# Kernel optimization log

Measured on AMD Instinct MI355X. Metric: run time of the kernel, lower is better.

The kernel has to match this reference:

```python
import jax, jax.numpy as jnp
import numpy as np

MASK_VALUE = -1000000.0  # matches torch source's value=-1000000.0


def setup_inputs() -> dict:
    key = jax.random.key(0)
    kq, kk, kv, kl = jax.random.split(key, 4)
    B, S, D = 64, 1024, 64
    q = jax.random.normal(kq, (B, S, D), dtype=jnp.float32)
    k = jax.random.normal(kk, (B, S, D), dtype=jnp.float32)
    v = jax.random.normal(kv, (B, S, D), dtype=jnp.float32)
    valid_lens = jax.random.randint(kl, (B,), 0, S, dtype=jnp.int32)
    return {"q": q, "k": k, "v": v, "valid_lens": valid_lens}


def reference(q, k, v, valid_lens):
    # scores: [B, Sq, Sk]
    d = q.shape[-1]
    scores = jnp.einsum("bqd,bkd->bqk", q, k) / jnp.sqrt(jnp.float32(d))
    # 1-D valid_lens broadcast over the query dim (torch repeat_interleave branch)
    Sk = k.shape[1]
    mask = jnp.arange(Sk, dtype=jnp.int32)[None, None, :] < valid_lens[:, None, None]
    scores = jnp.where(mask, scores, MASK_VALUE)
    attn = jax.nn.softmax(scores, axis=-1)
    # dropout p=0.0 -> identity (eval-mode reference)
    return jnp.einsum("bqk,bkd->bqd", attn, v)
```

## Files before the change

kernel.cpp:

```cpp
#include <hip/hip_runtime.h>
#include <math.h>


#define BATCH 64
#define SEQ   1024
#define DIM   64
#define BQ    64
#define BC    64
#define NKT   (SEQ / BC)
#define LSTR  72
#define QSCALE 0.18033688011112442f
#define MASKED -1.0e6f

typedef __attribute__((ext_vector_type(8))) short bf16x8;
typedef __attribute__((ext_vector_type(4))) float f32x4;

__device__ __forceinline__ uint pack2_trunc(float lo, float hi) {
    return __builtin_amdgcn_perm(__float_as_uint(hi), __float_as_uint(lo), 0x07060302);
}
__device__ __forceinline__ ushort f2bf_rne(float x) {
    uint u = __float_as_uint(x);
    return (ushort)((u + 0x7fffu + ((u >> 16) & 1u)) >> 16);
}

__global__ __launch_bounds__(256, 4) void attn_mfma_flash2(
    const float* __restrict__ q, const float* __restrict__ k,
    const float* __restrict__ v, const int* __restrict__ valid_lens,
    float* __restrict__ out)
{
    __shared__ ushort Ks[BC * LSTR];
    __shared__ ushort Vt[DIM * LSTR];
    __shared__ ushort Ps[BQ * LSTR];

    const int t    = threadIdx.x;
    const int wave = t >> 6;
    const int wl   = t & 63;
    const int QD   = wl >> 4;
    const int li   = wl & 15;
    const int b    = blockIdx.x & 63;
    const int q0   = (blockIdx.x >> 6) * BQ;
    const int vl   = valid_lens[b];

    const size_t boff = (size_t)b * SEQ * DIM;

    bf16x8 qb[2];
    {
        const float* qrow = q + boff + (size_t)(q0 + wave * 16 + li) * DIM + QD * 8;
        #pragma unroll
        for (int kc = 0; kc < 2; kc++) {
            float4 a = *(const float4*)(qrow + kc * 32);
            float4 c = *(const float4*)(qrow + kc * 32 + 4);
            union { bf16x8 v; ushort u[8]; } tmp;
            tmp.u[0] = f2bf_rne(a.x * QSCALE);
            tmp.u[1] = f2bf_rne(a.y * QSCALE);
            tmp.u[2] = f2bf_rne(a.z * QSCALE);
            tmp.u[3] = f2bf_rne(a.w * QSCALE);
            tmp.u[4] = f2bf_rne(c.x * QSCALE);
            tmp.u[5] = f2bf_rne(c.y * QSCALE);
            tmp.u[6] = f2bf_rne(c.z * QSCALE);
            tmp.u[7] = f2bf_rne(c.w * QSCALE);
            qb[kc] = tmp.v;
        }
    }

    const int it_max = (vl == 0) ? NKT : ((vl + BC - 1) >> 6);

    float4 kf[4];
    float  vf[2][8];

    auto load_tile = [&](int it) {
        const float4* kg = (const float4*)(k + boff + (size_t)it * BC * DIM);
        #pragma unroll
        for (int i = 0; i < 4; i++) kf[i] = kg[t + 256 * i];
        const float* vgf = v + boff + (size_t)it * BC * DIM;
        #pragma unroll
        for (int i = 0; i < 2; i++) {
            int slot = t + 256 * i;
            int d = slot & 63, ko = slot >> 6;
            #pragma unroll
            for (int j = 0; j < 8; j++)
                vf[i][j] = vgf[(size_t)(ko * 8 + j) * DIM + d];
        }
    };

    auto stage = [&]() {
        #pragma unroll
        for (int i = 0; i < 4; i++) {
            int idx = t + 256 * i;
            int row = idx >> 4, c4 = idx & 15;
            uint2 w;
            w.x = pack2_trunc(kf[i].x, kf[i].y);
            w.y = pack2_trunc(kf[i].z, kf[i].w);
            *(uint2*)&Ks[row * LSTR + c4 * 4] = w;
        }
        #pragma unroll
        for (int i = 0; i < 2; i++) {
            int slot = t + 256 * i;
            int d = slot & 63, ko = slot >> 6;
            uint4 w;
            w.x = pack2_trunc(vf[i][0], vf[i][1]);
            w.y = pack2_trunc(vf[i][2], vf[i][3]);
            w.z = pack2_trunc(vf[i][4], vf[i][5]);
            w.w = pack2_trunc(vf[i][6], vf[i][7]);
            *(uint4*)&Vt[d * LSTR + ko * 8] = w;
        }
    };

    float m_run = -INFINITY, l_run = 0.f;
    f32x4 acc[4];
    #pragma unroll
    for (int dt = 0; dt < 4; dt++) acc[dt] = (f32x4){0.f, 0.f, 0.f, 0.f};

    load_tile(0);

    for (int it = 0; it < it_max; it++) {
        __syncthreads();
        stage();
        if (it + 1 < it_max) load_tile(it + 1);
        __syncthreads();

        f32x4 sc[4];
        #pragma unroll
        for (int kt = 0; kt < 4; kt++) {
            bf16x8 ka0 = *(const bf16x8*)&Ks[(kt * 16 + li) * LSTR + QD * 8];
            bf16x8 ka1 = *(const bf16x8*)&Ks[(kt * 16 + li) * LSTR + 32 + QD * 8];
            f32x4 c = (f32x4){0.f, 0.f, 0.f, 0.f};
            c = __builtin_amdgcn_mfma_f32_16x16x32_bf16(ka0, qb[0], c, 0, 0, 0);
            c = __builtin_amdgcn_mfma_f32_16x16x32_bf16(ka1, qb[1], c, 0, 0, 0);
            sc[kt] = c;
        }

        const int kbase = it * BC;
        if (kbase + BC > vl) {
            #pragma unroll
            for (int kt = 0; kt < 4; kt++)
                #pragma unroll
                for (int r = 0; r < 4; r++) {
                    int key = kbase + kt * 16 + QD * 4 + r;
                    if (key >= vl) sc[kt][r] = MASKED;
                }
        }

        float mt = -INFINITY;
        #pragma unroll
        for (int kt = 0; kt < 4; kt++)
            #pragma unroll
            for (int r = 0; r < 4; r++) mt = fmaxf(mt, sc[kt][r]);
        mt = fmaxf(mt, __shfl_xor(mt, 16, 64));
        mt = fmaxf(mt, __shfl_xor(mt, 32, 64));
        float mn = fmaxf(m_run, mt);
        float alpha = exp2f(m_run - mn);
        m_run = mn;

        float ls = 0.f;
        #pragma unroll
        for (int kt = 0; kt < 4; kt++) {
            float p0 = exp2f(sc[kt][0] - mn);
            float p1 = exp2f(sc[kt][1] - mn);
            float p2 = exp2f(sc[kt][2] - mn);
            float p3 = exp2f(sc[kt][3] - mn);
            ls += (p0 + p1) + (p2 + p3);
            uint2 w;
            w.x = pack2_trunc(p0, p1);
            w.y = pack2_trunc(p2, p3);
            *(uint2*)&Ps[(wave * 16 + li) * LSTR + kt * 16 + QD * 4] = w;
        }
        ls += __shfl_xor(ls, 16, 64);
        ls += __shfl_xor(ls, 32, 64);
        l_run = l_run * alpha + ls;

        float a0 = __shfl(alpha, QD * 4 + 0, 64);
        float a1 = __shfl(alpha, QD * 4 + 1, 64);
        float a2 = __shfl(alpha, QD * 4 + 2, 64);
        float a3 = __shfl(alpha, QD * 4 + 3, 64);
        #pragma unroll
        for (int dt = 0; dt < 4; dt++) {
            acc[dt][0] *= a0; acc[dt][1] *= a1;
            acc[dt][2] *= a2; acc[dt][3] *= a3;
        }

        bf16x8 pa0 = *(const bf16x8*)&Ps[(wave * 16 + li) * LSTR + QD * 8];
        bf16x8 pa1 = *(const bf16x8*)&Ps[(wave * 16 + li) * LSTR + 32 + QD * 8];
        #pragma unroll
        for (int dt = 0; dt < 4; dt++) {
            bf16x8 vb0 = *(const bf16x8*)&Vt[(dt * 16 + li) * LSTR + QD * 8];
            bf16x8 vb1 = *(const bf16x8*)&Vt[(dt * 16 + li) * LSTR + 32 + QD * 8];
            acc[dt] = __builtin_amdgcn_mfma_f32_16x16x32_bf16(pa0, vb0, acc[dt], 0, 0, 0);
            acc[dt] = __builtin_amdgcn_mfma_f32_16x16x32_bf16(pa1, vb1, acc[dt], 0, 0, 0);
        }
    }

    float invl = 1.0f / l_run;
    float i0 = __shfl(invl, QD * 4 + 0, 64);
    float i1 = __shfl(invl, QD * 4 + 1, 64);
    float i2 = __shfl(invl, QD * 4 + 2, 64);
    float i3 = __shfl(invl, QD * 4 + 3, 64);
    float* ob = out + boff + (size_t)q0 * DIM;
    const int rbase = wave * 16 + QD * 4;
    #pragma unroll
    for (int dt = 0; dt < 4; dt++) {
        int col = dt * 16 + li;
        ob[(size_t)(rbase + 0) * DIM + col] = acc[dt][0] * i0;
        ob[(size_t)(rbase + 1) * DIM + col] = acc[dt][1] * i1;
        ob[(size_t)(rbase + 2) * DIM + col] = acc[dt][2] * i2;
        ob[(size_t)(rbase + 3) * DIM + col] = acc[dt][3] * i3;
    }
}

extern "C" void kernel_launch(void* const* d_in, const int* in_sizes, int n_in,
                              void* d_out, int out_size, void* d_ws, size_t ws_size,
                              hipStream_t stream) {
    const float* q = (const float*)d_in[0];
    const float* k = (const float*)d_in[1];
    const float* v = (const float*)d_in[2];
    const int* valid_lens = (const int*)d_in[3];
    float* out = (float*)d_out;

    dim3 grid(BATCH * (SEQ / BQ));
    dim3 block(256);
    attn_mfma_flash2<<<grid, block, 0, stream>>>(q, k, v, valid_lens, out);
}
```

Baseline: 127.5 us.

## Use persistent blocks with atomic work queue and smaller double-buffered key tiles

The kernel becomes persistent: 768 blocks pull (batch, query-tile) items from a global atomic counter instead of launching one block per item. This balances the uneven per-batch work that variable valid_lens creates. The key tile shrinks from 64 to 32, and K/V fragments are read into registers before the barrier so the next tile can be staged while MFMAs run, giving a two-deep prefetch. The cost is an extra memset launch, the atomic traffic, more barriers per key, and lower occupancy from launch bounds of 3.

```diff
diff --git a/kernel.cpp b/kernel.cpp
--- a/kernel.cpp
+++ b/kernel.cpp
@@ -6,9 +6,13 @@
 #define SEQ   1024
 #define DIM   64
 #define BQ    64
-#define BC    64
+#define BC    32
 #define NKT   (SEQ / BC)
-#define LSTR  72
+#define KSTR  72
+#define VSTR  40
+#define PSTR  40
+#define NITEMS (BATCH * (SEQ / BQ))
+#define GRID  768
 #define QSCALE 0.18033688011112442f
 #define MASKED -1.0e6f
 
@@ -23,187 +27,191 @@
     return (ushort)((u + 0x7fffu + ((u >> 16) & 1u)) >> 16);
 }
 
-__global__ __launch_bounds__(256, 4) void attn_mfma_flash2(
+__global__ __launch_bounds__(256, 3) void attn_mfma_flash4(
     const float* __restrict__ q, const float* __restrict__ k,
     const float* __restrict__ v, const int* __restrict__ valid_lens,
-    float* __restrict__ out)
+    float* __restrict__ out, unsigned* __restrict__ cnt)
 {
-    __shared__ ushort Ks[BC * LSTR];
-    __shared__ ushort Vt[DIM * LSTR];
-    __shared__ ushort Ps[BQ * LSTR];
+    __shared__ ushort Ks[BC * KSTR];
+    __shared__ ushort Vt[DIM * VSTR];
+    __shared__ ushort Ps[BQ * PSTR];
+    __shared__ int next_item;
 
     const int t    = threadIdx.x;
     const int wave = t >> 6;
     const int wl   = t & 63;
     const int QD   = wl >> 4;
     const int li   = wl & 15;
-    const int b    = blockIdx.x & 63;
-    const int q0   = (blockIdx.x >> 6) * BQ;
-    const int vl   = valid_lens[b];
-
-    const size_t boff = (size_t)b * SEQ * DIM;
-
-    bf16x8 qb[2];
-    {
-        const float* qrow = q + boff + (size_t)(q0 + wave * 16 + li) * DIM + QD * 8;
+
+    int item = blockIdx.x;
+    while (item < NITEMS) {
+        const int b  = item & 63;
+        const int q0 = (item >> 6) * BQ;
+        const int vl = valid_lens[b];
+        const size_t boff = (size_t)b * SEQ * DIM;
+
+        bf16x8 qb[2];
+        {
+            const float* qrow = q + boff + (size_t)(q0 + wave * 16 + li) * DIM + QD * 8;
+            #pragma unroll
+            for (int kc = 0; kc < 2; kc++) {
+                float4 a = *(const float4*)(qrow + kc * 32);
+                float4 c = *(const float4*)(qrow + kc * 32 + 4);
+                union { bf16x8 v; ushort u[8]; } tmp;
+                tmp.u[0] = f2bf_rne(a.x * QSCALE);
+                tmp.u[1] = f2bf_rne(a.y * QSCALE);
+                tmp.u[2] = f2bf_rne(a.z * QSCALE);
+                tmp.u[3] = f2bf_rne(a.w * QSCALE);
+                tmp.u[4] = f2bf_rne(c.x * QSCALE);
+                tmp.u[5] = f2bf_rne(c.y * QSCALE);
+                tmp.u[6] = f2bf_rne(c.z * QSCALE);
+                tmp.u[7] = f2bf_rne(c.w * QSCALE);
+                qb[kc] = tmp.v;
+            }
+        }
+
+        const int it_max = (vl == 0) ? NKT : ((vl + BC - 1) / BC);
+
+        float4 kf[2];
+        float  vf[8];
+
+        auto load_tile = [&](int it) {
+            const float4* kg = (const float4*)(k + boff + (size_t)it * BC * DIM);
+            kf[0] = kg[t];
+            kf[1] = kg[t + 256];
+            const float* vgf = v + boff + (size_t)it * BC * DIM;
+            #pragma unroll
+            for (int j = 0; j < 8; j++)
+                vf[j] = vgf[(size_t)(wave * 8 + j) * DIM + wl];
+        };
+        auto stage = [&]() {
+            #pragma unroll
+            for (int i = 0; i < 2; i++) {
+                int idx = t + 256 * i;
+                int row = idx >> 4, c4 = idx & 15;
+                uint2 w;
+                w.x = pack2_trunc(kf[i].x, kf[i].y);
+                w.y = pack2_trunc(kf[i].z, kf[i].w);
+                *(uint2*)&Ks[row * KSTR + c4 * 4] = w;
+            }
+            uint4 wv;
+            wv.x = pack2_trunc(vf[0], vf[1]);
+            wv.y = pack2_trunc(vf[2], vf[3]);
+            wv.z = pack2_trunc(vf[4], vf[5]);
+            wv.w = pack2_trunc(vf[6], vf[7]);
+            *(uint4*)&Vt[wl * VSTR + wave * 8] = wv;
+        };
+
+        float m_run = -INFINITY, l_run = 0.f;
+        f32x4 acc[4];
         #pragma unroll
-        for (int kc = 0; kc < 2; kc++) {
-            float4 a = *(const float4*)(qrow + kc * 32);
-            float4 c = *(const float4*)(qrow + kc * 32 + 4);
-            union { bf16x8 v; ushort u[8]; } tmp;
-            tmp.u[0] = f2bf_rne(a.x * QSCALE);
-            tmp.u[1] = f2bf_rne(a.y * QSCALE);
-            tmp.u[2] = f2bf_rne(a.z * QSCALE);
-            tmp.u[3] = f2bf_rne(a.w * QSCALE);
-            tmp.u[4] = f2bf_rne(c.x * QSCALE);
-            tmp.u[5] = f2bf_rne(c.y * QSCALE);
-            tmp.u[6] = f2bf_rne(c.z * QSCALE);
-            tmp.u[7] = f2bf_rne(c.w * QSCALE);
-            qb[kc] = tmp.v;
+        for (int dt = 0; dt < 4; dt++) acc[dt] = (f32x4){0.f, 0.f, 0.f, 0.f};
+
+        load_tile(0);
+        stage();
+        if (it_max > 1) load_tile(1);
+        __syncthreads();
+
+        for (int it = 0; it < it_max; it++) {
+            bf16x8 ka[2][2], vb[4];
+            #pragma unroll
+            for (int kt = 0; kt < 2; kt++) {
+                ka[kt][0] = *(const bf16x8*)&Ks[(kt * 16 + li) * KSTR + QD * 8];
+                ka[kt][1] = *(const bf16x8*)&Ks[(kt * 16 + li) * KSTR + 32 + QD * 8];
+            }
+            #pragma unroll
+            for (int dt = 0; dt < 4; dt++)
+                vb[dt] = *(const bf16x8*)&Vt[(dt * 16 + li) * VSTR + QD * 8];
+            __syncthreads();
+
+            if (it + 1 < it_max) stage();
+            if (it + 2 < it_max) load_tile(it + 2);
+
+            f32x4 sc[2];
+            #pragma unroll
+            for (int kt = 0; kt < 2; kt++) {
+                f32x4 c = (f32x4){0.f, 0.f, 0.f, 0.f};
+                c = __builtin_amdgcn_mfma_f32_16x16x32_bf16(ka[kt][0], qb[0], c, 0, 0, 0);
+                c = __builtin_amdgcn_mfma_f32_16x16x32_bf16(ka[kt][1], qb[1], c, 0, 0, 0);
+                sc[kt] = c;
+            }
+
+            const int kbase = it * BC;
+            if (kbase + BC > vl) {
+                #pragma unroll
+                for (int kt = 0; kt < 2; kt++)
+                    #pragma unroll
+                    for (int r = 0; r < 4; r++) {
+                        int key = kbase + kt * 16 + QD * 4 + r;
+                        if (key >= vl) sc[kt][r] = MASKED;
+                    }
+            }
+
+            float mt = -INFINITY;
+            #pragma unroll
+            for (int kt = 0; kt < 2; kt++)
+                #pragma unroll
+                for (int r = 0; r < 4; r++) mt = fmaxf(mt, sc[kt][r]);
+            mt = fmaxf(mt, __shfl_xor(mt, 16, 64));
+            mt = fmaxf(mt, __shfl_xor(mt, 32, 64));
+            float mn = fmaxf(m_run, mt);
+            float alpha = exp2f(m_run - mn);
+            m_run = mn;
+
+            float ls = 0.f;
+            #pragma unroll
+            for (int kt = 0; kt < 2; kt++) {
+                float p0 = exp2f(sc[kt][0] - mn);
+                float p1 = exp2f(sc[kt][1] - mn);
+                float p2 = exp2f(sc[kt][2] - mn);
+                float p3 = exp2f(sc[kt][3] - mn);
+                ls += (p0 + p1) + (p2 + p3);
+                uint2 w;
+                w.x = pack2_trunc(p0, p1);
+                w.y = pack2_trunc(p2, p3);
+                *(uint2*)&Ps[(wave * 16 + li) * PSTR + kt * 16 + QD * 4] = w;
+            }
+            ls += __shfl_xor(ls, 16, 64);
+            ls += __shfl_xor(ls, 32, 64);
+            l_run = l_run * alpha + ls;
+
+            float a0 = __shfl(alpha, QD * 4 + 0, 64);
+            float a1 = __shfl(alpha, QD * 4 + 1, 64);
+            float a2 = __shfl(alpha, QD * 4 + 2, 64);
+            float a3 = __shfl(alpha, QD * 4 + 3, 64);
+            #pragma unroll
+            for (int dt = 0; dt < 4; dt++) {
+                acc[dt][0] *= a0; acc[dt][1] *= a1;
+                acc[dt][2] *= a2; acc[dt][3] *= a3;
+            }
+
+            bf16x8 pa = *(const bf16x8*)&Ps[(wave * 16 + li) * PSTR + QD * 8];
+            #pragma unroll
+            for (int dt = 0; dt < 4; dt++)
+                acc[dt] = __builtin_amdgcn_mfma_f32_16x16x32_bf16(pa, vb[dt], acc[dt], 0, 0, 0);
+
+            __syncthreads();
         }
-    }
-
-    const int it_max = (vl == 0) ? NKT : ((vl + BC - 1) >> 6);
-
-    float4 kf[4];
-    float  vf[2][8];
-
-    auto load_tile = [&](int it) {
-        const float4* kg = (const float4*)(k + boff + (size_t)it * BC * DIM);
-        #pragma unroll
-        for (int i = 0; i < 4; i++) kf[i] = kg[t + 256 * i];
-        const float* vgf = v + boff + (size_t)it * BC * DIM;
-        #pragma unroll
-        for (int i = 0; i < 2; i++) {
-            int slot = t + 256 * i;
-            int d = slot & 63, ko = slot >> 6;
-            #pragma unroll
-            for (int j = 0; j < 8; j++)
-                vf[i][j] = vgf[(size_t)(ko * 8 + j) * DIM + d];
-        }
-    };
-
-    auto stage = [&]() {
-        #pragma unroll
-        for (int i = 0; i < 4; i++) {
-            int idx = t + 256 * i;
-            int row = idx >> 4, c4 = idx & 15;
-            uint2 w;
-            w.x = pack2_trunc(kf[i].x, kf[i].y);
-            w.y = pack2_trunc(kf[i].z, kf[i].w);
-            *(uint2*)&Ks[row * LSTR + c4 * 4] = w;
-        }
-        #pragma unroll
-        for (int i = 0; i < 2; i++) {
-            int slot = t + 256 * i;
-            int d = slot & 63, ko = slot >> 6;
-            uint4 w;
-            w.x = pack2_trunc(vf[i][0], vf[i][1]);
-            w.y = pack2_trunc(vf[i][2], vf[i][3]);
-            w.z = pack2_trunc(vf[i][4], vf[i][5]);
-            w.w = pack2_trunc(vf[i][6], vf[i][7]);
-            *(uint4*)&Vt[d * LSTR + ko * 8] = w;
-        }
-    };
-
-    float m_run = -INFINITY, l_run = 0.f;
-    f32x4 acc[4];
-    #pragma unroll
-    for (int dt = 0; dt < 4; dt++) acc[dt] = (f32x4){0.f, 0.f, 0.f, 0.f};
-
-    load_tile(0);
-
-    for (int it = 0; it < it_max; it++) {
-        __syncthreads();
-        stage();
-        if (it + 1 < it_max) load_tile(it + 1);
-        __syncthreads();
-
-        f32x4 sc[4];
-        #pragma unroll
-        for (int kt = 0; kt < 4; kt++) {
-            bf16x8 ka0 = *(const bf16x8*)&Ks[(kt * 16 + li) * LSTR + QD * 8];
-            bf16x8 ka1 = *(const bf16x8*)&Ks[(kt * 16 + li) * LSTR + 32 + QD * 8];
-            f32x4 c = (f32x4){0.f, 0.f, 0.f, 0.f};
-            c = __builtin_amdgcn_mfma_f32_16x16x32_bf16(ka0, qb[0], c, 0, 0, 0);
-            c = __builtin_amdgcn_mfma_f32_16x16x32_bf16(ka1, qb[1], c, 0, 0, 0);
-            sc[kt] = c;
-        }
-
-        const int kbase = it * BC;
-        if (kbase + BC > vl) {
-            #pragma unroll
-            for (int kt = 0; kt < 4; kt++)
-                #pragma unroll
-                for (int r = 0; r < 4; r++) {
-                    int key = kbase + kt * 16 + QD * 4 + r;
-                    if (key >= vl) sc[kt][r] = MASKED;
-                }
-        }
-
-        float mt = -INFINITY;
-        #pragma unroll
-        for (int kt = 0; kt < 4; kt++)
-            #pragma unroll
-            for (int r = 0; r < 4; r++) mt = fmaxf(mt, sc[kt][r]);
-        mt = fmaxf(mt, __shfl_xor(mt, 16, 64));
-        mt = fmaxf(mt, __shfl_xor(mt, 32, 64));
-        float mn = fmaxf(m_run, mt);
-        float alpha = exp2f(m_run - mn);
-        m_run = mn;
-
-        float ls = 0.f;
-        #pragma unroll
-        for (int kt = 0; kt < 4; kt++) {
-            float p0 = exp2f(sc[kt][0] - mn);
-            float p1 = exp2f(sc[kt][1] - mn);
-            float p2 = exp2f(sc[kt][2] - mn);
-            float p3 = exp2f(sc[kt][3] - mn);
-            ls += (p0 + p1) + (p2 + p3);
-            uint2 w;
-            w.x = pack2_trunc(p0, p1);
-            w.y = pack2_trunc(p2, p3);
-            *(uint2*)&Ps[(wave * 16 + li) * LSTR + kt * 16 + QD * 4] = w;
-        }
-        ls += __shfl_xor(ls, 16, 64);
-        ls += __shfl_xor(ls, 32, 64);
-        l_run = l_run * alpha + ls;
-
-        float a0 = __shfl(alpha, QD * 4 + 0, 64);
-        float a1 = __shfl(alpha, QD * 4 + 1, 64);
-        float a2 = __shfl(alpha, QD * 4 + 2, 64);
-        float a3 = __shfl(alpha, QD * 4 + 3, 64);
+
+        float invl = 1.0f / l_run;
+        float i0 = __shfl(invl, QD * 4 + 0, 64);
+        float i1 = __shfl(invl, QD * 4 + 1, 64);
+        float i2 = __shfl(invl, QD * 4 + 2, 64);
+        float i3 = __shfl(invl, QD * 4 + 3, 64);
+        float* ob = out + boff + (size_t)q0 * DIM;
+        const int rbase = wave * 16 + QD * 4;
         #pragma unroll
         for (int dt = 0; dt < 4; dt++) {
-            acc[dt][0] *= a0; acc[dt][1] *= a1;
-            acc[dt][2] *= a2; acc[dt][3] *= a3;
+            int col = dt * 16 + li;
+            ob[(size_t)(rbase + 0) * DIM + col] = acc[dt][0] * i0;
+            ob[(size_t)(rbase + 1) * DIM + col] = acc[dt][1] * i1;
+            ob[(size_t)(rbase + 2) * DIM + col] = acc[dt][2] * i2;
+            ob[(size_t)(rbase + 3) * DIM + col] = acc[dt][3] * i3;
         }
 
-        bf16x8 pa0 = *(const bf16x8*)&Ps[(wave * 16 + li) * LSTR + QD * 8];
-        bf16x8 pa1 = *(const bf16x8*)&Ps[(wave * 16 + li) * LSTR + 32 + QD * 8];
-        #pragma unroll
-        for (int dt = 0; dt < 4; dt++) {
-            bf16x8 vb0 = *(const bf16x8*)&Vt[(dt * 16 + li) * LSTR + QD * 8];
-            bf16x8 vb1 = *(const bf16x8*)&Vt[(dt * 16 + li) * LSTR + 32 + QD * 8];
-            acc[dt] = __builtin_amdgcn_mfma_f32_16x16x32_bf16(pa0, vb0, acc[dt], 0, 0, 0);
-            acc[dt] = __builtin_amdgcn_mfma_f32_16x16x32_bf16(pa1, vb1, acc[dt], 0, 0, 0);
-        }
-    }
-
-    float invl = 1.0f / l_run;
-    float i0 = __shfl(invl, QD * 4 + 0, 64);
-    float i1 = __shfl(invl, QD * 4 + 1, 64);
-    float i2 = __shfl(invl, QD * 4 + 2, 64);
-    float i3 = __shfl(invl, QD * 4 + 3, 64);
-    float* ob = out + boff + (size_t)q0 * DIM;
-    const int rbase = wave * 16 + QD * 4;
-    #pragma unroll
-    for (int dt = 0; dt < 4; dt++) {
-        int col = dt * 16 + li;
-        ob[(size_t)(rbase + 0) * DIM + col] = acc[dt][0] * i0;
-        ob[(size_t)(rbase + 1) * DIM + col] = acc[dt][1] * i1;
-        ob[(size_t)(rbase + 2) * DIM + col] = acc[dt][2] * i2;
-        ob[(size_t)(rbase + 3) * DIM + col] = acc[dt][3] * i3;
+        if (t == 0) next_item = GRID + (int)atomicAdd(cnt, 1u);
+        __syncthreads();
+        item = next_item;
     }
 }
 
@@ -215,8 +223,8 @@
     const float* v = (const float*)d_in[2];
     const int* valid_lens = (const int*)d_in[3];
     float* out = (float*)d_out;
-
-    dim3 grid(BATCH * (SEQ / BQ));
-    dim3 block(256);
-    attn_mfma_flash2<<<grid, block, 0, stream>>>(q, k, v, valid_lens, out);
-}
+    unsigned* cnt = (unsigned*)d_ws;
+
+    hipMemsetAsync(cnt, 0, sizeof(unsigned), stream);
+    attn_mfma_flash4<<<dim3(GRID), dim3(256), 0, stream>>>(q, k, v, valid_lens, out, cnt);
+}
```

Result: slower. 135.4 us (+6.2%).
